# Optimization experiments

Hardware: AMD Instinct MI355X
Metric: run time of the kernel (lower is better)

The kernel has to match this reference:

```python
import jax, jax.numpy as jnp
import numpy as np

B, S, D, H = 4, 2048, 1024, 16
DEPTH = D // H  # 64


def setup_inputs() -> dict:
    key = jax.random.key(0)
    ks = jax.random.split(key, 11)
    scale = 1.0 / np.sqrt(D)
    inp = {
        "v": jax.random.normal(ks[0], (B, S, D), jnp.float32),
        "k": jax.random.normal(ks[1], (B, S, D), jnp.float32),
        "q": jax.random.normal(ks[2], (B, S, D), jnp.float32),
        # causal mask: 1.0 where attention is disallowed (strict upper triangle)
        "mask": jnp.triu(jnp.ones((S, S), jnp.float32), k=1)[None, None, :, :],
        "wq": jax.random.normal(ks[3], (D, D), jnp.float32) * scale,
        "bq": jnp.zeros((D,), jnp.float32),
        "wk": jax.random.normal(ks[4], (D, D), jnp.float32) * scale,
        "bk": jnp.zeros((D,), jnp.float32),
        "wv": jax.random.normal(ks[5], (D, D), jnp.float32) * scale,
        "bv": jnp.zeros((D,), jnp.float32),
        "wo": jax.random.normal(ks[6], (D, D), jnp.float32) * scale,
        "bo": jnp.zeros((D,), jnp.float32),
    }
    return inp


def _split_heads(x):
    # [B, S, D] -> [B, H, S, depth]
    b, s, _ = x.shape
    return x.reshape(b, s, H, DEPTH).transpose(0, 2, 1, 3)


def reference(v, k, q, mask, wq, bq, wk, bk, wv, bv, wo, bo):
    qh = _split_heads(q @ wq + bq)  # [B,H,S,depth]
    kh = _split_heads(k @ wk + bk)
    vh = _split_heads(v @ wv + bv)

    logits = jnp.einsum("bhqd,bhkd->bhqk", qh, kh) / jnp.sqrt(
        jnp.asarray(DEPTH, jnp.float32)
    )
    logits = logits + mask * -1e9
    attn = jax.nn.softmax(logits, axis=-1)  # [B,H,S,S]
    out = jnp.einsum("bhqk,bhkd->bhqd", attn, vh)
    out = out.transpose(0, 2, 1, 3).reshape(q.shape[0], -1, D)  # [B,S,D]
    return out @ wo + bo
```

## Files before the change

kernel.cpp:

```cpp
#include <hip/hip_runtime.h>

typedef _Float16 f16;
typedef _Float16 half8 __attribute__((ext_vector_type(8)));
typedef _Float16 half4v __attribute__((ext_vector_type(4)));
typedef _Float16 half2v __attribute__((ext_vector_type(2)));
typedef float f32x4 __attribute__((ext_vector_type(4)));

__device__ __forceinline__ void gl_lds16(const void* g, void* l) {
    __builtin_amdgcn_global_load_lds((const __attribute__((address_space(1))) void*)g,
                                     (__attribute__((address_space(3))) void*)l, 16, 0, 0);
}

__device__ __forceinline__ unsigned pack_f16(float a, float b) {
    union { half2v h; unsigned u; } un;
    un.h[0] = (f16)a; un.h[1] = (f16)b;
    return un.u;
}

__global__ __launch_bounds__(256) void cvt_f32_f16(const float* __restrict__ x, f16* __restrict__ y)
{
    const size_t i = ((size_t)blockIdx.x * 256 + threadIdx.x) * 8;
    const float4 a = *(const float4*)(x + i);
    const float4 b = *(const float4*)(x + i + 4);
    half8 h;
    h[0] = (f16)a.x; h[1] = (f16)a.y; h[2] = (f16)a.z; h[3] = (f16)a.w;
    h[4] = (f16)b.x; h[5] = (f16)b.y; h[6] = (f16)b.z; h[7] = (f16)b.w;
    *(half8*)(y + i) = h;
}

__device__ __forceinline__ void prep_w_body(const float* __restrict__ W, f16* __restrict__ Wt)
{
    __shared__ float t[64][65];
    const int tid = threadIdx.x;
    const int tk = blockIdx.x * 64, tn = blockIdx.y * 64;
    const int rr = tid >> 4, cc = (tid & 15) * 4;
    #pragma unroll
    for (int j = 0; j < 4; ++j) {
        float4 v = *(const float4*)(W + (size_t)(tk + rr + j * 16) * 1024 + tn + cc);
        t[rr + j * 16][cc] = v.x; t[rr + j * 16][cc + 1] = v.y;
        t[rr + j * 16][cc + 2] = v.z; t[rr + j * 16][cc + 3] = v.w;
    }
    __syncthreads();
    const int n = tid >> 2, kc = (tid & 3) * 16;
    f16 o[16];
    #pragma unroll
    for (int j = 0; j < 16; ++j) o[j] = (f16)t[kc + j][n];
    f16* dst = Wt + (size_t)(tn + n) * 1024 + tk + kc;
    *(uint4*)dst = *(uint4*)o;
    *(uint4*)(dst + 8) = *(uint4*)(o + 8);
}

__global__ __launch_bounds__(256) void prep_w1(const float* __restrict__ W, f16* __restrict__ Wt)
{ prep_w_body(W, Wt); }

__global__ __launch_bounds__(256) void prep_w3(const float* __restrict__ w0,
    const float* __restrict__ w1, const float* __restrict__ w2, f16* __restrict__ Wt)
{
    const int z = blockIdx.z;
    const float* W = (z == 0) ? w0 : (z == 1) ? w1 : w2;
    prep_w_body(W, Wt + (size_t)z * 1024 * 1024);
}

template<int OUT>
__global__ __launch_bounds__(256, 2) void gemm_kernel(
    const f16* __restrict__ X, const f16* __restrict__ Wt,
    const float* __restrict__ bias, void* __restrict__ outv)
{
    __shared__ __align__(16) f16 As[3][128 * 32];
    __shared__ __align__(16) f16 Bs[3][128 * 32];

    const int tid = threadIdx.x;
    const int lane = tid & 63;
    const int lane16 = lane & 15, quad = lane >> 4;
    const int wave = tid >> 6;
    const int wm = (wave >> 1) * 64, wn = (wave & 1) * 64;

    const int lin = blockIdx.x + 8 * blockIdx.y;
    const int xcd = lin & 7, t = lin >> 3;
    const int m0 = ((t >> 3) * 8 + xcd) * 128;
    const int n0 = (t & 7) * 128;

    const int wbase = tid & 192;
    const int l2 = lane16 & 3;
    const int srow = tid >> 2, schunk = tid & 3;

    f32x4 acc[4][4] = {};

    #pragma unroll
    for (int pt = 0; pt < 2; ++pt)
        #pragma unroll
        for (int i = 0; i < 2; ++i) {
            const int row = i * 64 + srow;
            const int sw = (schunk ^ (row & 3)) * 8;
            gl_lds16(Wt + (size_t)(n0 + row) * 1024 + pt * 32 + sw, Bs[pt] + (size_t)(i * 256 + wbase) * 8);
            gl_lds16(X  + (size_t)(m0 + row) * 1024 + pt * 32 + sw, As[pt] + (size_t)(i * 256 + wbase) * 8);
        }

    int cur = 0;
    for (int kt = 0; kt < 32; ++kt) {
        if (kt + 2 < 32) {
            const int nx2 = (cur >= 1) ? cur - 1 : 2;
            const int k2 = (kt + 2) * 32;
            #pragma unroll
            for (int i = 0; i < 2; ++i) {
                const int row = i * 64 + srow;
                const int sw = (schunk ^ (row & 3)) * 8;
                gl_lds16(Wt + (size_t)(n0 + row) * 1024 + k2 + sw, Bs[nx2] + (size_t)(i * 256 + wbase) * 8);
                gl_lds16(X  + (size_t)(m0 + row) * 1024 + k2 + sw, As[nx2] + (size_t)(i * 256 + wbase) * 8);
            }
            asm volatile("s_waitcnt vmcnt(8)" ::: "memory");
        } else if (kt + 1 < 32) {
            asm volatile("s_waitcnt vmcnt(4)" ::: "memory");
        } else {
            asm volatile("s_waitcnt vmcnt(0)" ::: "memory");
        }
        __builtin_amdgcn_s_barrier();
        asm volatile("" ::: "memory");

        half8 af[4], bf[4];
        #pragma unroll
        for (int i = 0; i < 4; ++i)
            af[i] = *(const half8*)(As[cur] + (wm + i * 16 + lane16) * 32 + ((quad ^ l2) * 8));
        #pragma unroll
        for (int i = 0; i < 4; ++i)
            bf[i] = *(const half8*)(Bs[cur] + (wn + i * 16 + lane16) * 32 + ((quad ^ l2) * 8));
        #pragma unroll
        for (int mi = 0; mi < 4; ++mi)
            #pragma unroll
            for (int ni = 0; ni < 4; ++ni)
                acc[mi][ni] = __builtin_amdgcn_mfma_f32_16x16x32_f16(af[mi], bf[ni], acc[mi][ni], 0, 0, 0);

        asm volatile("" ::: "memory");
        __builtin_amdgcn_s_barrier();
        asm volatile("" ::: "memory");
        cur = (cur == 2) ? 0 : cur + 1;
    }

    #pragma unroll
    for (int mi = 0; mi < 4; ++mi) {
        #pragma unroll
        for (int ni = 0; ni < 4; ++ni) {
            const int col = n0 + wn + ni * 16 + lane16;
            const float bval = bias[col];
            const int grow0 = m0 + wm + mi * 16 + quad * 4;
            if (OUT == 2) {
                const int b = grow0 >> 11, s0 = grow0 & 2047;
                const int h = col >> 6, d = col & 63;
                half4v p;
                #pragma unroll
                for (int r = 0; r < 4; ++r) p[r] = (f16)(acc[mi][ni][r] + bval);
                *(half4v*)((f16*)outv + (((size_t)b * 16 + h) * 64 + d) * 2048 + s0) = p;
            } else if (OUT == 0) {
                #pragma unroll
                for (int r = 0; r < 4; ++r)
                    ((f16*)outv)[(size_t)(grow0 + r) * 1024 + col] = (f16)(acc[mi][ni][r] + bval);
            } else {
                #pragma unroll
                for (int r = 0; r < 4; ++r)
                    ((float*)outv)[(size_t)(grow0 + r) * 1024 + col] = acc[mi][ni][r] + bval;
            }
        }
    }
}

__global__ __launch_bounds__(256, 2) void attn_kernel(
    const f16* __restrict__ qh, const f16* __restrict__ kh,
    const f16* __restrict__ vt, f16* __restrict__ at)
{
    __shared__ __align__(16) f16 Ks[3][64 * 64];
    __shared__ __align__(16) f16 Vts[3][64 * 64];

    const int tid = threadIdx.x;
    const int lane = tid & 63, wave = tid >> 6;
    const int lane16 = lane & 15, quad = lane >> 4;
    const int wbase = tid & 192;
    const int l3 = lane16 & 7;
    const int srow = tid >> 3, schunk = tid & 7;

    const int lin = blockIdx.x + 8 * blockIdx.y;
    const int xcd = lin & 7, t = lin >> 3;
    const int bh = xcd + 8 * (t & 7);
    const int bx = t >> 3;
    const int b = bh >> 4, h = bh & 15;

    const f16* qp = qh + (size_t)b * 2048 * 1024 + h * 64;
    const f16* kp = kh + (size_t)b * 2048 * 1024 + h * 64;
    const f16* vtp = vt + (size_t)bh * 64 * 2048;

    for (int pass = 0; pass < 2; ++pass) {
        const int qb = 128 * (pass == 0 ? (15 - bx) : bx);
        const int qrow0 = qb + wave * 32;
        const int ntiles = qb / 64 + 2;
        const int qmax = qrow0 + 31;

        #pragma unroll
        for (int pt = 0; pt < 2; ++pt)
            #pragma unroll
            for (int i = 0; i < 2; ++i) {
                const int row = i * 32 + srow;
                const int sw = (schunk ^ (row & 7)) * 8;
                gl_lds16(kp + (size_t)(pt * 64 + row) * 1024 + sw, Ks[pt] + (size_t)(i * 256 + wbase) * 8);
                gl_lds16(vtp + (size_t)row * 2048 + pt * 64 + sw, Vts[pt] + (size_t)(i * 256 + wbase) * 8);
            }

        half8 aq[2][2];
        #pragma unroll
        for (int mt = 0; mt < 2; ++mt)
            #pragma unroll
            for (int c = 0; c < 2; ++c)
                aq[mt][c] = *(const half8*)(qp + (size_t)(qrow0 + mt * 16 + lane16) * 1024 + c * 32 + quad * 8);

        f32x4 o[4][2] = {};
        float lp[2] = {0.0f, 0.0f};

        int cur = 0;
        for (int kt = 0; kt < ntiles; ++kt) {
            if (kt + 2 < ntiles) {
                const int nx2 = (cur >= 1) ? cur - 1 : 2;
                const int k2 = (kt + 2) * 64;
                #pragma unroll
                for (int i = 0; i < 2; ++i) {
                    const int row = i * 32 + srow;
                    const int sw = (schunk ^ (row & 7)) * 8;
                    gl_lds16(kp + (size_t)(k2 + row) * 1024 + sw, Ks[nx2] + (size_t)(i * 256 + wbase) * 8);
                    gl_lds16(vtp + (size_t)row * 2048 + k2 + sw, Vts[nx2] + (size_t)(i * 256 + wbase) * 8);
                }
                asm volatile("s_waitcnt vmcnt(8)" ::: "memory");
            } else if (kt + 1 < ntiles) {
                asm volatile("s_waitcnt vmcnt(4)" ::: "memory");
            } else {
                asm volatile("s_waitcnt vmcnt(0)" ::: "memory");
            }
            __builtin_amdgcn_s_barrier();
            asm volatile("" ::: "memory");

            const int k0 = kt * 64;
            if (k0 <= qmax) {
                f32x4 sT[4][2];
                #pragma unroll
                for (int sub = 0; sub < 4; ++sub) {
                    const int kr = sub * 16 + lane16;
                    const half8 ak0 = *(const half8*)(Ks[cur] + kr * 64 + ((quad ^ l3) * 8));
                    const half8 ak1 = *(const half8*)(Ks[cur] + kr * 64 + (((4 + quad) ^ l3) * 8));
                    #pragma unroll
                    for (int mt = 0; mt < 2; ++mt) {
                        f32x4 z = {};
                        z = __builtin_amdgcn_mfma_f32_16x16x32_f16(ak0, aq[mt][0], z, 0, 0, 0);
                        z = __builtin_amdgcn_mfma_f32_16x16x32_f16(ak1, aq[mt][1], z, 0, 0, 0);
                        sT[sub][mt] = z;
                    }
                }
                const bool needmask = (k0 + 63 > qrow0);
                if (needmask) {
                    #pragma unroll
                    for (int sub = 0; sub < 4; ++sub)
                        #pragma unroll
                        for (int mt = 0; mt < 2; ++mt)
                            #pragma unroll
                            for (int r = 0; r < 4; ++r) {
                                const int key = k0 + sub * 16 + quad * 4 + r;
                                const int qi = qrow0 + mt * 16 + lane16;
                                if (key > qi) sT[sub][mt][r] = -1e30f;
                            }
                }

                half8 bp[2][2];
                #pragma unroll
                for (int mt = 0; mt < 2; ++mt) {
                    unsigned pk01[4], pk23[4];
                    #pragma unroll
                    for (int sub = 0; sub < 4; ++sub) {
                        float p[4];
                        #pragma unroll
                        for (int r = 0; r < 4; ++r) {
                            const float x = fmaf(sT[sub][mt][r], 0.18033688011112042f, -5.770780163555852f);
                            float e;
                            asm("v_exp_f32 %0, %1" : "=v"(e) : "v"(x));
                            p[r] = e;
                            lp[mt] += e;
                        }
                        pk01[sub] = pack_f16(p[0], p[1]);
                        pk23[sub] = pack_f16(p[2], p[3]);
                    }
                    #pragma unroll
                    for (int c = 0; c < 2; ++c) {
                        unsigned a0 = pk01[2 * c], b0 = pk01[2 * c + 1];
                        unsigned a1 = pk23[2 * c], b1 = pk23[2 * c + 1];
                        asm("v_permlane32_swap_b32 %0, %1" : "+v"(a0), "+v"(b0));
                        asm("v_permlane16_swap_b32 %0, %1" : "+v"(a0), "+v"(b0));
                        asm("v_permlane32_swap_b32 %0, %1" : "+v"(a1), "+v"(b1));
                        asm("v_permlane16_swap_b32 %0, %1" : "+v"(a1), "+v"(b1));
                        union { unsigned u[4]; half8 h8; } un;
                        un.u[0] = a0; un.u[1] = a1; un.u[2] = b0; un.u[3] = b1;
                        bp[c][mt] = un.h8;
                    }
                }

                #pragma unroll
                for (int nt = 0; nt < 4; ++nt) {
                    const int dr = nt * 16 + lane16;
                    const half8 av0 = *(const half8*)(Vts[cur] + dr * 64 + ((quad ^ l3) * 8));
                    const half8 av1 = *(const half8*)(Vts[cur] + dr * 64 + (((4 + quad) ^ l3) * 8));
                    #pragma unroll
                    for (int mt = 0; mt < 2; ++mt) {
                        o[nt][mt] = __builtin_amdgcn_mfma_f32_16x16x32_f16(av0, bp[0][mt], o[nt][mt], 0, 0, 0);
                        o[nt][mt] = __builtin_amdgcn_mfma_f32_16x16x32_f16(av1, bp[1][mt], o[nt][mt], 0, 0, 0);
                    }
                }
            }
            asm volatile("" ::: "memory");
            __builtin_amdgcn_s_barrier();
            asm volatile("" ::: "memory");
            cur = (cur == 2) ? 0 : cur + 1;
        }

        #pragma unroll
        for (int mt = 0; mt < 2; ++mt) {
            float red = lp[mt];
            red += __shfl_xor(red, 16);
            red += __shfl_xor(red, 32);
            const float inv = 1.0f / red;
            const int sr = qrow0 + mt * 16 + lane16;
            f16* dst = at + ((size_t)b * 2048 + sr) * 1024 + h * 64 + quad * 4;
            #pragma unroll
            for (int nt = 0; nt < 4; ++nt) {
                half4v p;
                #pragma unroll
                for (int r = 0; r < 4; ++r) p[r] = (f16)(o[nt][mt][r] * inv);
                *(half4v*)(dst + nt * 16) = p;
            }
        }
    }
}

extern "C" void kernel_launch(void* const* d_in, const int* in_sizes, int n_in,
                              void* d_out, int out_size, void* d_ws, size_t ws_size,
                              hipStream_t stream)
{
    const float* v  = (const float*)d_in[0];
    const float* k  = (const float*)d_in[1];
    const float* q  = (const float*)d_in[2];
    const float* wq = (const float*)d_in[4];
    const float* bq = (const float*)d_in[5];
    const float* wk = (const float*)d_in[6];
    const float* bk = (const float*)d_in[7];
    const float* wv = (const float*)d_in[8];
    const float* bv = (const float*)d_in[9];
    const float* wo = (const float*)d_in[10];
    const float* bo = (const float*)d_in[11];

    f16* qh = (f16*)d_ws;
    f16* kh = qh + (size_t)8 * 1024 * 1024;
    f16* vt = kh + (size_t)8 * 1024 * 1024;
    f16* at = vt + (size_t)8 * 1024 * 1024;

    f16* wT = (f16*)d_out;
    f16* wqT = wT;
    f16* wkT = wT + (size_t)1024 * 1024;
    f16* wvT = wT + (size_t)2 * 1024 * 1024;
    f16* xf  = wT + (size_t)3 * 1024 * 1024;
    f16* woT = qh;

    prep_w3<<<dim3(16, 16, 3), 256, 0, stream>>>(wq, wk, wv, wT);

    dim3 g(8, 64);
    cvt_f32_f16<<<4096, 256, 0, stream>>>(q, xf);
    gemm_kernel<0><<<g, 256, 0, stream>>>(xf, wqT, bq, qh);
    cvt_f32_f16<<<4096, 256, 0, stream>>>(k, xf);
    gemm_kernel<0><<<g, 256, 0, stream>>>(xf, wkT, bk, kh);
    cvt_f32_f16<<<4096, 256, 0, stream>>>(v, xf);
    gemm_kernel<2><<<g, 256, 0, stream>>>(xf, wvT, bv, vt);

    attn_kernel<<<dim3(8, 64), 256, 0, stream>>>(qh, kh, vt, at);

    prep_w1<<<dim3(16, 16), 256, 0, stream>>>(wo, woT);
    gemm_kernel<1><<<g, 256, 0, stream>>>(at, woT, bo, d_out);
}
```

Baseline: 335.9 us.

## Double-buffer GEMM with BK=64 and split attention passes into separate blocks

The GEMM moves from a triple-buffered BK=32 pipeline to a double-buffered BK=64 pipeline with an 8-way XOR swizzle, which halves the barrier count per K and doubles the MFMA work per stage. The attention kernel drops its two-pass balanced loop, where one block handled a long and a short query tile. It now launches twice as many blocks, one query tile each, with double buffering and launch bounds raised to 4 blocks per CU for occupancy. This gives up the explicit causal load balancing within a block and relies on the scheduler, processing heavy tiles first.

```diff
diff --git a/kernel.cpp b/kernel.cpp
--- a/kernel.cpp
+++ b/kernel.cpp
@@ -66,8 +66,8 @@
     const f16* __restrict__ X, const f16* __restrict__ Wt,
     const float* __restrict__ bias, void* __restrict__ outv)
 {
-    __shared__ __align__(16) f16 As[3][128 * 32];
-    __shared__ __align__(16) f16 Bs[3][128 * 32];
+    __shared__ __align__(16) f16 As[2][128 * 64];
+    __shared__ __align__(16) f16 Bs[2][128 * 64];
 
     const int tid = threadIdx.x;
     const int lane = tid & 63;
@@ -81,59 +81,60 @@
     const int n0 = (t & 7) * 128;
 
     const int wbase = tid & 192;
-    const int l2 = lane16 & 3;
-    const int srow = tid >> 2, schunk = tid & 3;
+    const int srow = tid >> 3, schunk = tid & 7;
 
     f32x4 acc[4][4] = {};
 
     #pragma unroll
-    for (int pt = 0; pt < 2; ++pt)
-        #pragma unroll
-        for (int i = 0; i < 2; ++i) {
-            const int row = i * 64 + srow;
-            const int sw = (schunk ^ (row & 3)) * 8;
-            gl_lds16(Wt + (size_t)(n0 + row) * 1024 + pt * 32 + sw, Bs[pt] + (size_t)(i * 256 + wbase) * 8);
-            gl_lds16(X  + (size_t)(m0 + row) * 1024 + pt * 32 + sw, As[pt] + (size_t)(i * 256 + wbase) * 8);
-        }
-
-    int cur = 0;
-    for (int kt = 0; kt < 32; ++kt) {
-        if (kt + 2 < 32) {
-            const int nx2 = (cur >= 1) ? cur - 1 : 2;
-            const int k2 = (kt + 2) * 32;
-            #pragma unroll
-            for (int i = 0; i < 2; ++i) {
-                const int row = i * 64 + srow;
-                const int sw = (schunk ^ (row & 3)) * 8;
-                gl_lds16(Wt + (size_t)(n0 + row) * 1024 + k2 + sw, Bs[nx2] + (size_t)(i * 256 + wbase) * 8);
-                gl_lds16(X  + (size_t)(m0 + row) * 1024 + k2 + sw, As[nx2] + (size_t)(i * 256 + wbase) * 8);
+    for (int i = 0; i < 4; ++i) {
+        const int row = i * 32 + srow;
+        const int sw = (schunk ^ (row & 7)) * 8;
+        gl_lds16(Wt + (size_t)(n0 + row) * 1024 + sw, Bs[0] + (size_t)(i * 256 + wbase) * 8);
+        gl_lds16(X  + (size_t)(m0 + row) * 1024 + sw, As[0] + (size_t)(i * 256 + wbase) * 8);
+    }
+
+    for (int kt = 0; kt < 16; ++kt) {
+        if (kt + 1 < 16) {
+            const int nb = (kt + 1) & 1;
+            const int k1 = (kt + 1) * 64;
+            #pragma unroll
+            for (int i = 0; i < 4; ++i) {
+                const int row = i * 32 + srow;
+                const int sw = (schunk ^ (row & 7)) * 8;
+                gl_lds16(Wt + (size_t)(n0 + row) * 1024 + k1 + sw, Bs[nb] + (size_t)(i * 256 + wbase) * 8);
+                gl_lds16(X  + (size_t)(m0 + row) * 1024 + k1 + sw, As[nb] + (size_t)(i * 256 + wbase) * 8);
             }
             asm volatile("s_waitcnt vmcnt(8)" ::: "memory");
-        } else if (kt + 1 < 32) {
-            asm volatile("s_waitcnt vmcnt(4)" ::: "memory");
         } else {
             asm volatile("s_waitcnt vmcnt(0)" ::: "memory");
         }
         __builtin_amdgcn_s_barrier();
         asm volatile("" ::: "memory");
 
-        half8 af[4], bf[4];
-        #pragma unroll
-        for (int i = 0; i < 4; ++i)
-            af[i] = *(const half8*)(As[cur] + (wm + i * 16 + lane16) * 32 + ((quad ^ l2) * 8));
-        #pragma unroll
-        for (int i = 0; i < 4; ++i)
-            bf[i] = *(const half8*)(Bs[cur] + (wn + i * 16 + lane16) * 32 + ((quad ^ l2) * 8));
-        #pragma unroll
-        for (int mi = 0; mi < 4; ++mi)
-            #pragma unroll
-            for (int ni = 0; ni < 4; ++ni)
-                acc[mi][ni] = __builtin_amdgcn_mfma_f32_16x16x32_f16(af[mi], bf[ni], acc[mi][ni], 0, 0, 0);
+        const f16* Ab = As[kt & 1];
+        const f16* Bb = Bs[kt & 1];
+        half8 af[4][2], bf[4][2];
+        #pragma unroll
+        for (int i = 0; i < 4; ++i) {
+            const int ra = wm + i * 16 + lane16;
+            const int rb = wn + i * 16 + lane16;
+            #pragma unroll
+            for (int c = 0; c < 2; ++c) {
+                af[i][c] = *(const half8*)(Ab + ra * 64 + (((c * 4 + quad) ^ (ra & 7)) * 8));
+                bf[i][c] = *(const half8*)(Bb + rb * 64 + (((c * 4 + quad) ^ (rb & 7)) * 8));
+            }
+        }
+        #pragma unroll
+        for (int c = 0; c < 2; ++c)
+            #pragma unroll
+            for (int mi = 0; mi < 4; ++mi)
+                #pragma unroll
+                for (int ni = 0; ni < 4; ++ni)
+                    acc[mi][ni] = __builtin_amdgcn_mfma_f32_16x16x32_f16(af[mi][c], bf[ni][c], acc[mi][ni], 0, 0, 0);
 
         asm volatile("" ::: "memory");
         __builtin_amdgcn_s_barrier();
         asm volatile("" ::: "memory");
-        cur = (cur == 2) ? 0 : cur + 1;
     }
 
     #pragma unroll
@@ -163,12 +164,12 @@
     }
 }
 
-__global__ __launch_bounds__(256, 2) void attn_kernel(
+__global__ __launch_bounds__(256, 4) void attn_kernel(
     const f16* __restrict__ qh, const f16* __restrict__ kh,
     const f16* __restrict__ vt, f16* __restrict__ at)
 {
-    __shared__ __align__(16) f16 Ks[3][64 * 64];
-    __shared__ __align__(16) f16 Vts[3][64 * 64];
+    __shared__ __align__(16) f16 Ks[2][64 * 64];
+    __shared__ __align__(16) f16 Vts[2][64 * 64];
 
     const int tid = threadIdx.x;
     const int lane = tid & 63, wave = tid >> 6;
@@ -177,158 +178,152 @@
     const int l3 = lane16 & 7;
     const int srow = tid >> 3, schunk = tid & 7;
 
-    const int lin = blockIdx.x + 8 * blockIdx.y;
+    const int lin = blockIdx.x + 16 * blockIdx.y;
     const int xcd = lin & 7, t = lin >> 3;
     const int bh = xcd + 8 * (t & 7);
-    const int bx = t >> 3;
+    const int qi = 15 - (t >> 3);
     const int b = bh >> 4, h = bh & 15;
 
     const f16* qp = qh + (size_t)b * 2048 * 1024 + h * 64;
     const f16* kp = kh + (size_t)b * 2048 * 1024 + h * 64;
     const f16* vtp = vt + (size_t)bh * 64 * 2048;
 
-    for (int pass = 0; pass < 2; ++pass) {
-        const int qb = 128 * (pass == 0 ? (15 - bx) : bx);
-        const int qrow0 = qb + wave * 32;
-        const int ntiles = qb / 64 + 2;
-        const int qmax = qrow0 + 31;
-
-        #pragma unroll
-        for (int pt = 0; pt < 2; ++pt)
+    const int qb = 128 * qi;
+    const int qrow0 = qb + wave * 32;
+    const int ntiles = qb / 64 + 2;
+    const int qmax = qrow0 + 31;
+
+    #pragma unroll
+    for (int i = 0; i < 2; ++i) {
+        const int row = i * 32 + srow;
+        const int sw = (schunk ^ (row & 7)) * 8;
+        gl_lds16(kp + (size_t)row * 1024 + sw, Ks[0] + (size_t)(i * 256 + wbase) * 8);
+        gl_lds16(vtp + (size_t)row * 2048 + sw, Vts[0] + (size_t)(i * 256 + wbase) * 8);
+    }
+
+    half8 aq[2][2];
+    #pragma unroll
+    for (int mt = 0; mt < 2; ++mt)
+        #pragma unroll
+        for (int c = 0; c < 2; ++c)
+            aq[mt][c] = *(const half8*)(qp + (size_t)(qrow0 + mt * 16 + lane16) * 1024 + c * 32 + quad * 8);
+
+    f32x4 o[4][2] = {};
+    float lp[2] = {0.0f, 0.0f};
+
+    for (int kt = 0; kt < ntiles; ++kt) {
+        if (kt + 1 < ntiles) {
+            const int nb = (kt + 1) & 1;
+            const int k1 = (kt + 1) * 64;
             #pragma unroll
             for (int i = 0; i < 2; ++i) {
                 const int row = i * 32 + srow;
                 const int sw = (schunk ^ (row & 7)) * 8;
-                gl_lds16(kp + (size_t)(pt * 64 + row) * 1024 + sw, Ks[pt] + (size_t)(i * 256 + wbase) * 8);
-                gl_lds16(vtp + (size_t)row * 2048 + pt * 64 + sw, Vts[pt] + (size_t)(i * 256 + wbase) * 8);
-            }
-
-        half8 aq[2][2];
-        #pragma unroll
-        for (int mt = 0; mt < 2; ++mt)
-            #pragma unroll
-            for (int c = 0; c < 2; ++c)
-                aq[mt][c] = *(const half8*)(qp + (size_t)(qrow0 + mt * 16 + lane16) * 1024 + c * 32 + quad * 8);
-
-        f32x4 o[4][2] = {};
-        float lp[2] = {0.0f, 0.0f};
-
-        int cur = 0;
-        for (int kt = 0; kt < ntiles; ++kt) {
-            if (kt + 2 < ntiles) {
-                const int nx2 = (cur >= 1) ? cur - 1 : 2;
-                const int k2 = (kt + 2) * 64;
-                #pragma unroll
-                for (int i = 0; i < 2; ++i) {
-                    const int row = i * 32 + srow;
-                    const int sw = (schunk ^ (row & 7)) * 8;
-                    gl_lds16(kp + (size_t)(k2 + row) * 1024 + sw, Ks[nx2] + (size_t)(i * 256 + wbase) * 8);
-                    gl_lds16(vtp + (size_t)row * 2048 + k2 + sw, Vts[nx2] + (size_t)(i * 256 + wbase) * 8);
+                gl_lds16(kp + (size_t)(k1 + row) * 1024 + sw, Ks[nb] + (size_t)(i * 256 + wbase) * 8);
+                gl_lds16(vtp + (size_t)row * 2048 + k1 + sw, Vts[nb] + (size_t)(i * 256 + wbase) * 8);
+            }
+            asm volatile("s_waitcnt vmcnt(4)" ::: "memory");
+        } else {
+            asm volatile("s_waitcnt vmcnt(0)" ::: "memory");
+        }
+        __builtin_amdgcn_s_barrier();
+        asm volatile("" ::: "memory");
+
+        const int k0 = kt * 64;
+        if (k0 <= qmax) {
+            const f16* Kb = Ks[kt & 1];
+            const f16* Vb = Vts[kt & 1];
+            f32x4 sT[4][2];
+            #pragma unroll
+            for (int sub = 0; sub < 4; ++sub) {
+                const int kr = sub * 16 + lane16;
+                const half8 ak0 = *(const half8*)(Kb + kr * 64 + ((quad ^ l3) * 8));
+                const half8 ak1 = *(const half8*)(Kb + kr * 64 + (((4 + quad) ^ l3) * 8));
+                #pragma unroll
+                for (int mt = 0; mt < 2; ++mt) {
+                    f32x4 z = {};
+                    z = __builtin_amdgcn_mfma_f32_16x16x32_f16(ak0, aq[mt][0], z, 0, 0, 0);
+                    z = __builtin_amdgcn_mfma_f32_16x16x32_f16(ak1, aq[mt][1], z, 0, 0, 0);
+                    sT[sub][mt] = z;
                 }
-                asm volatile("s_waitcnt vmcnt(8)" ::: "memory");
-            } else if (kt + 1 < ntiles) {
-                asm volatile("s_waitcnt vmcnt(4)" ::: "memory");
-            } else {
-                asm volatile("s_waitcnt vmcnt(0)" ::: "memory");
-            }
-            __builtin_amdgcn_s_barrier();
-            asm volatile("" ::: "memory");
-
-            const int k0 = kt * 64;
-            if (k0 <= qmax) {
-                f32x4 sT[4][2];
-                #pragma unroll
-                for (int sub = 0; sub < 4; ++sub) {
-                    const int kr = sub * 16 + lane16;
-                    const half8 ak0 = *(const half8*)(Ks[cur] + kr * 64 + ((quad ^ l3) * 8));
-                    const half8 ak1 = *(const half8*)(Ks[cur] + kr * 64 + (((4 + quad) ^ l3) * 8));
+            }
+            const bool needmask = (k0 + 63 > qrow0);
+            if (needmask) {
+                #pragma unroll
+                for (int sub = 0; sub < 4; ++sub)
                     #pragma unroll
-                    for (int mt = 0; mt < 2; ++mt) {
-                        f32x4 z = {};
-                        z = __builtin_amdgcn_mfma_f32_16x16x32_f16(ak0, aq[mt][0], z, 0, 0, 0);
-                        z = __builtin_amdgcn_mfma_f32_16x16x32_f16(ak1, aq[mt][1], z, 0, 0, 0);
-                        sT[sub][mt] = z;
-                    }
-                }
-                const bool needmask = (k0 + 63 > qrow0);
-                if (needmask) {
-                    #pragma unroll
-                    for (int sub = 0; sub < 4; ++sub)
-                        #pragma unroll
-                        for (int mt = 0; mt < 2; ++mt)
-                            #pragma unroll
-                            for (int r = 0; r < 4; ++r) {
-                                const int key = k0 + sub * 16 + quad * 4 + r;
-                                const int qi = qrow0 + mt * 16 + lane16;
-                                if (key > qi) sT[sub][mt][r] = -1e30f;
-                            }
-                }
-
-                half8 bp[2][2];
-                #pragma unroll
-                for (int mt = 0; mt < 2; ++mt) {
-                    unsigned pk01[4], pk23[4];
-                    #pragma unroll
-                    for (int sub = 0; sub < 4; ++sub) {
-                        float p[4];
+                    for (int mt = 0; mt < 2; ++mt)
                         #pragma unroll
                         for (int r = 0; r < 4; ++r) {
-                            const float x = fmaf(sT[sub][mt][r], 0.18033688011112042f, -5.770780163555852f);
-                            float e;
-                            asm("v_exp_f32 %0, %1" : "=v"(e) : "v"(x));
-                            p[r] = e;
-                            lp[mt] += e;
+                            const int key = k0 + sub * 16 + quad * 4 + r;
+                            const int qi2 = qrow0 + mt * 16 + lane16;
+                            if (key > qi2) sT[sub][mt][r] = -1e30f;
                         }
-                        pk01[sub] = pack_f16(p[0], p[1]);
-                        pk23[sub] = pack_f16(p[2], p[3]);
+            }
+
+            half8 bp[2][2];
+            #pragma unroll
+            for (int mt = 0; mt < 2; ++mt) {
+                unsigned pk01[4], pk23[4];
+                #pragma unroll
+                for (int sub = 0; sub < 4; ++sub) {
+                    float p[4];
+                    #pragma unroll
+                    for (int r = 0; r < 4; ++r) {
+                        const float x = fmaf(sT[sub][mt][r], 0.18033688011112042f, -5.770780163555852f);
+                        float e;
+                        asm("v_exp_f32 %0, %1" : "=v"(e) : "v"(x));
+                        p[r] = e;
+                        lp[mt] += e;
                     }
-                    #pragma unroll
-                    for (int c = 0; c < 2; ++c) {
-                        unsigned a0 = pk01[2 * c], b0 = pk01[2 * c + 1];
-                        unsigned a1 = pk23[2 * c], b1 = pk23[2 * c + 1];
-                        asm("v_permlane32_swap_b32 %0, %1" : "+v"(a0), "+v"(b0));
-                        asm("v_permlane16_swap_b32 %0, %1" : "+v"(a0), "+v"(b0));
-                        asm("v_permlane32_swap_b32 %0, %1" : "+v"(a1), "+v"(b1));
-                        asm("v_permlane16_swap_b32 %0, %1" : "+v"(a1), "+v"(b1));
-                        union { unsigned u[4]; half8 h8; } un;
-                        un.u[0] = a0; un.u[1] = a1; un.u[2] = b0; un.u[3] = b1;
-                        bp[c][mt] = un.h8;
-                    }
+                    pk01[sub] = pack_f16(p[0], p[1]);
+                    pk23[sub] = pack_f16(p[2], p[3]);
                 }
-
-                #pragma unroll
-                for (int nt = 0; nt < 4; ++nt) {
-                    const int dr = nt * 16 + lane16;
-                    const half8 av0 = *(const half8*)(Vts[cur] + dr * 64 + ((quad ^ l3) * 8));
-                    const half8 av1 = *(const half8*)(Vts[cur] + dr * 64 + (((4 + quad) ^ l3) * 8));
-                    #pragma unroll
-                    for (int mt = 0; mt < 2; ++mt) {
-                        o[nt][mt] = __builtin_amdgcn_mfma_f32_16x16x32_f16(av0, bp[0][mt], o[nt][mt], 0, 0, 0);
-                        o[nt][mt] = __builtin_amdgcn_mfma_f32_16x16x32_f16(av1, bp[1][mt], o[nt][mt], 0, 0, 0);
-                    }
+                #pragma unroll
+                for (int c = 0; c < 2; ++c) {
+                    unsigned a0 = pk01[2 * c], b0 = pk01[2 * c + 1];
+                    unsigned a1 = pk23[2 * c], b1 = pk23[2 * c + 1];
+                    asm("v_permlane32_swap_b32 %0, %1" : "+v"(a0), "+v"(b0));
+                    asm("v_permlane16_swap_b32 %0, %1" : "+v"(a0), "+v"(b0));
+                    asm("v_permlane32_swap_b32 %0, %1" : "+v"(a1), "+v"(b1));
+                    asm("v_permlane16_swap_b32 %0, %1" : "+v"(a1), "+v"(b1));
+                    union { unsigned u[4]; half8 h8; } un;
+                    un.u[0] = a0; un.u[1] = a1; un.u[2] = b0; un.u[3] = b1;
+                    bp[c][mt] = un.h8;
                 }
             }
-            asm volatile("" ::: "memory");
-            __builtin_amdgcn_s_barrier();
-            asm volatile("" ::: "memory");
-            cur = (cur == 2) ? 0 : cur + 1;
-        }
-
-        #pragma unroll
-        for (int mt = 0; mt < 2; ++mt) {
-            float red = lp[mt];
-            red += __shfl_xor(red, 16);
-            red += __shfl_xor(red, 32);
-            const float inv = 1.0f / red;
-            const int sr = qrow0 + mt * 16 + lane16;
-            f16* dst = at + ((size_t)b * 2048 + sr) * 1024 + h * 64 + quad * 4;
+
             #pragma unroll
             for (int nt = 0; nt < 4; ++nt) {
-                half4v p;
-                #pragma unroll
-                for (int r = 0; r < 4; ++r) p[r] = (f16)(o[nt][mt][r] * inv);
-                *(half4v*)(dst + nt * 16) = p;
-            }
+                const int dr = nt * 16 + lane16;
+                const half8 av0 = *(const half8*)(Vb + dr * 64 + ((quad ^ l3) * 8));
+                const half8 av1 = *(const half8*)(Vb + dr * 64 + (((4 + quad) ^ l3) * 8));
+                #pragma unroll
+                for (int mt = 0; mt < 2; ++mt) {
+                    o[nt][mt] = __builtin_amdgcn_mfma_f32_16x16x32_f16(av0, bp[0][mt], o[nt][mt], 0, 0, 0);
+                    o[nt][mt] = __builtin_amdgcn_mfma_f32_16x16x32_f16(av1, bp[1][mt], o[nt][mt], 0, 0, 0);
+                }
+            }
+        }
+        asm volatile("" ::: "memory");
+        __builtin_amdgcn_s_barrier();
+        asm volatile("" ::: "memory");
+    }
+
+    #pragma unroll
+    for (int mt = 0; mt < 2; ++mt) {
+        float red = lp[mt];
+        red += __shfl_xor(red, 16);
+        red += __shfl_xor(red, 32);
+        const float inv = 1.0f / red;
+        const int sr = qrow0 + mt * 16 + lane16;
+        f16* dst = at + ((size_t)b * 2048 + sr) * 1024 + h * 64 + quad * 4;
+        #pragma unroll
+        for (int nt = 0; nt < 4; ++nt) {
+            half4v p;
+            #pragma unroll
+            for (int r = 0; r < 4; ++r) p[r] = (f16)(o[nt][mt][r] * inv);
+            *(half4v*)(dst + nt * 16) = p;
         }
     }
 }
@@ -371,7 +366,7 @@
     cvt_f32_f16<<<4096, 256, 0, stream>>>(v, xf);
     gemm_kernel<2><<<g, 256, 0, stream>>>(xf, wvT, bv, vt);
 
-    attn_kernel<<<dim3(8, 64), 256, 0, stream>>>(qh, kh, vt, at);
+    attn_kernel<<<dim3(16, 64), 256, 0, stream>>>(qh, kh, vt, at);
 
     prep_w1<<<dim3(16, 16), 256, 0, stream>>>(wo, woT);
     gemm_kernel<1><<<g, 256, 0, stream>>>(at, woT, bo, d_out);
```

Result: faster. 313.3 us (-6.7%).
